# Kernel optimization log

Measured on AMD Instinct MI355X. Metric: run time of the kernel, lower is better.

Reference implementation:

```python
import jax, jax.numpy as jnp
import numpy as np

KS = 3
N = KS * KS  # 9 kernel taps
EPS = 1e-5
LEAK = 0.1


def _conv2d(x, w, b=None, stride=1, pad=1):
    out = jax.lax.conv_general_dilated(
        x, w, (stride, stride), [(pad, pad), (pad, pad)],
        dimension_numbers=('NCHW', 'OIHW', 'NCHW'))
    if b is not None:
        out = out + b[None, :, None, None]
    return out


def setup_inputs() -> dict:
    key = jax.random.key(0)
    k1, k2, k3, k4 = jax.random.split(key, 4)
    b, c_in, c_out, H, W = 4, 128, 256, 128, 128
    x = jax.random.normal(k1, (b, c_in, H, W), dtype=jnp.float32)
    # offset-predicting conv (torch inits it to zero; small random keeps
    # sampling near-grid but nontrivial)
    p_w = jax.random.normal(k2, (2 * N, c_in, KS, KS), dtype=jnp.float32) * 0.01
    p_b = jnp.zeros((2 * N,), dtype=jnp.float32)
    # main conv weight (bias=False in DeformConv2d)
    w_conv = jax.random.normal(k3, (c_out, c_in, KS, KS), dtype=jnp.float32) * 0.05
    gamma = jnp.ones((c_out,), dtype=jnp.float32)
    beta = jnp.zeros((c_out,), dtype=jnp.float32)
    return {"x": x, "p_w": p_w, "p_b": p_b, "w_conv": w_conv,
            "gamma": gamma, "beta": beta}


def reference(x, p_w, p_b, w_conv, gamma, beta):
    b, c, H, W = x.shape
    # offsets: (b, 2N, H, W); first N channels = x-offsets, last N = y-offsets
    off = jnp.transpose(_conv2d(x, p_w, p_b), (0, 2, 3, 1))  # (b,h,w,2N)
    off_x, off_y = off[..., :N], off[..., N:]

    x_pad = jnp.pad(x, ((0, 0), (0, 0), (1, 1), (1, 1)))  # zero_padding(1)
    Hp, Wp = H + 2, W + 2

    # p = p_0 + p_n + offset (in padded coordinates)
    dx = jnp.repeat(jnp.arange(-1, 2), KS).astype(x.dtype)  # (9,)
    dy = jnp.tile(jnp.arange(-1, 2), KS).astype(x.dtype)
    p0x = jnp.arange(1, H + 1, dtype=x.dtype)[None, :, None, None]
    p0y = jnp.arange(1, W + 1, dtype=x.dtype)[None, None, :, None]
    px = p0x + dx + off_x  # (b,h,w,N)
    py = p0y + dy + off_y

    fx, fy = jnp.floor(px), jnp.floor(py)
    qlt_x = jnp.clip(fx, 0, Hp - 1)
    qlt_y = jnp.clip(fy, 0, Wp - 1)
    qrb_x = jnp.clip(fx + 1, 0, Hp - 1)
    qrb_y = jnp.clip(fy + 1, 0, Wp - 1)

    pcx = jnp.clip(px, 0, Hp - 1)
    pcy = jnp.clip(py, 0, Wp - 1)

    # bilinear weights (matches original g_lt/g_rb/g_lb/g_rt)
    g_lt = (1 + (qlt_x - pcx)) * (1 + (qlt_y - pcy))
    g_rb = (1 - (qrb_x - pcx)) * (1 - (qrb_y - pcy))
    g_lb = (1 + (qlt_x - pcx)) * (1 - (qrb_y - pcy))
    g_rt = (1 - (qrb_x - pcx)) * (1 + (qlt_y - pcy))

    x_flat = x_pad.reshape(b, c, Hp * Wp)
    ilt_x, ilt_y = qlt_x.astype(jnp.int32), qlt_y.astype(jnp.int32)
    irb_x, irb_y = qrb_x.astype(jnp.int32), qrb_y.astype(jnp.int32)

    def samp(ix, iy, g):
        idx = (ix * Wp + iy).reshape(b, -1)  # (b, h*w*N)
        v = jnp.take_along_axis(x_flat, idx[:, None, :], axis=2)
        return g[:, None] * v.reshape(b, c, H, W, N)

    x_off = (samp(ilt_x, ilt_y, g_lt) + samp(irb_x, irb_y, g_rb)
             + samp(ilt_x, irb_y, g_lb) + samp(irb_x, ilt_y, g_rt))

    # equivalent to reshaping to (b,c,3h,3w) and conv(k=3,s=3), bias=False
    out = jnp.einsum('bchwn,ocn->bohw', x_off,
                     w_conv.reshape(w_conv.shape[0], c, N))

    # BatchNorm2d (training-mode batch stats, biased var) + LeakyReLU(0.1)
    mean = out.mean(axis=(0, 2, 3), keepdims=True)
    var = ((out - mean) ** 2).mean(axis=(0, 2, 3), keepdims=True)
    out = (out - mean) * jax.lax.rsqrt(var + EPS)
    out = out * gamma[None, :, None, None] + beta[None, :, None, None]
    return jnp.where(out >= 0, out, LEAK * out)
```

## Files before the change

### kernel.cpp

```cpp
#include <hip/hip_runtime.h>
#include <cstdint>

typedef __attribute__((ext_vector_type(8))) short bf16x8;
typedef __attribute__((ext_vector_type(4))) float f32x4;

#define B_   4
#define C_   128
#define H_   128
#define W_   128
#define HP_  130
#define WP_  130
#define O_   256
#define HW_  (H_*W_)

#define XPAD_BYTES   (B_*HP_*WP_*C_*2)
#define OFF_BYTE     XPAD_BYTES
#define OFF_BYTES    (B_*HW_*18*4)
#define WREPB_BYTE   (OFF_BYTE + OFF_BYTES)
#define WREPB_BYTES  (9*C_*O_*2)
#define STATS_BYTE   (WREPB_BYTE + WREPB_BYTES)
#define WOFF_BYTE    (STATS_BYTE + 4096)
#define WOFF_BYTES   (9*4*4*32*8*2)

typedef __attribute__((address_space(1))) const void gconst_void;
typedef __attribute__((address_space(3))) void lds_void;
#define GLD_LDS16(gp, lp) __builtin_amdgcn_global_load_lds((gconst_void*)(gp), (lds_void*)(lp), 16, 0, 0)

__device__ __forceinline__ unsigned pack_bf2(float a, float b) {
    unsigned ua = __builtin_bit_cast(unsigned, a) + 0x8000u;
    unsigned ub = __builtin_bit_cast(unsigned, b) + 0x8000u;
    return __builtin_amdgcn_perm(ub, ua, 0x07060302u);
}

__global__ void k_transpose(const float* __restrict__ x, unsigned short* __restrict__ xpad) {
    __shared__ float tile[32][33];
    int w0 = blockIdx.x * 32, c0 = blockIdx.y * 32;
    int bh = blockIdx.z;
    int b = bh >> 7, h = bh & 127;
    int tx = threadIdx.x, ty = threadIdx.y;
#pragma unroll
    for (int i = 0; i < 4; i++) {
        int c = c0 + ty + i * 8;
        tile[ty + i * 8][tx] = x[((b * C_ + c) * H_ + h) * W_ + w0 + tx];
    }
    __syncthreads();
    int tid = ty * 32 + tx;
    int cp = tid & 15;
    int wl = tid >> 4;
#pragma unroll
    for (int i = 0; i < 2; i++) {
        int wll = wl + i * 16;
        int w = w0 + wll;
        unsigned v = pack_bf2(tile[2 * cp][wll], tile[2 * cp + 1][wll]);
        *(unsigned*)(&xpad[((size_t)((b * HP_ + h + 1) * WP_ + (w + 1))) * C_ + c0 + 2 * cp]) = v;
    }
}

__global__ void k_repackA(const float* __restrict__ p_w, short* __restrict__ wofff,
                          const float* __restrict__ w_conv, unsigned short* __restrict__ wrepb) {
    int i = blockIdx.x * 256 + threadIdx.x;
    if (i < 9 * 4096) {
        int e = i & 7, m = (i >> 3) & 31, q = (i >> 8) & 3, kc = (i >> 10) & 3, tap = i >> 12;
        float f = (m < 18) ? p_w[((size_t)m * C_ + kc * 32 + q * 8 + e) * 9 + tap] : 0.f;
        unsigned u = __builtin_bit_cast(unsigned, f);
        u += 0x7fffu + ((u >> 16) & 1u);
        wofff[i] = (short)(u >> 16);
    }
    int j = i - 9 * 4096;
    if (j >= 0 && j < 9 * C_ * O_) {
        int ki8 = j & 7;
        int o   = (j >> 3) & 255;
        int kq  = (j >> 11) & 3;
        int kc  = (j >> 13) & 3;
        int n   = j >> 15;
        int c = kc * 32 + kq * 8 + ki8;
        float f = w_conv[(o * C_ + c) * 9 + n];
        unsigned u = __builtin_bit_cast(unsigned, f);
        u += 0x7fffu + ((u >> 16) & 1u);
        wrepb[j] = (unsigned short)(u >> 16);
    }
}

__global__ __launch_bounds__(256) void k_offconv(const unsigned short* __restrict__ xpad,
                                                 const short* __restrict__ wofff,
                                                 const float* __restrict__ p_b,
                                                 float* __restrict__ offT) {
    int t = threadIdx.x;
    int ph = blockIdx.x;
    int h  = blockIdx.y;
    int b  = blockIdx.z;
    const unsigned short* xb = xpad + (size_t)b * HP_ * WP_ * C_;
    int lane = t & 63, wv = t >> 6;
    int q = lane >> 4, l15 = lane & 15;
    int pos0 = ph * 64 + wv * 16;
    int poscol = pos0 + l15;

    f32x4 accA = {0.f, 0.f, 0.f, 0.f}, accB = {0.f, 0.f, 0.f, 0.f};
    const bf16x8* Wf = (const bf16x8*)wofff;

    for (int tap = 0; tap < 9; tap++) {
        int row = h + tap / 3;
        int col = poscol + tap % 3;
        const unsigned short* src = xb + ((size_t)(row * WP_ + col)) * C_ + q * 8;
#pragma unroll
        for (int kc = 0; kc < 4; kc++) {
            bf16x8 a0 = Wf[(size_t)(((tap * 4 + kc) * 4 + q) * 32) + l15];
            bf16x8 a1 = Wf[(size_t)(((tap * 4 + kc) * 4 + q) * 32) + 16 + l15];
            bf16x8 bv = *(const bf16x8*)(src + kc * 32);
            accA = __builtin_amdgcn_mfma_f32_16x16x32_bf16(a0, bv, accA, 0, 0, 0);
            accB = __builtin_amdgcn_mfma_f32_16x16x32_bf16(a1, bv, accB, 0, 0, 0);
        }
    }
    size_t hw = (size_t)h * W_ + pos0 + l15;
#pragma unroll
    for (int r = 0; r < 4; r++) {
        int j = q * 4 + r;
        offT[((size_t)(b * 18 + j)) * HW_ + hw] = accA[r] + p_b[j];
    }
    if (q == 0) {
#pragma unroll
        for (int r = 0; r < 2; r++) {
            int j = 16 + r;
            offT[((size_t)(b * 18 + j)) * HW_ + hw] = accB[r] + p_b[j];
        }
    }
}

__global__ __launch_bounds__(512, 4) void k_main(const unsigned short* __restrict__ xpad,
                                                 const float* __restrict__ offT,
                                                 const unsigned short* __restrict__ wrepb,
                                                 float* __restrict__ out,
                                                 float* __restrict__ stats) {
    __shared__ short Wl[2][8192];
    __shared__ short Vl[2][4128];
    __shared__ int   pbase[2][4][128];
    __shared__ float pg[2][4][128];
    __shared__ float red0[256], red1[256];

    int t = threadIdx.x;
    int i_blk = blockIdx.x;
    int b = i_blk & 3;
    int h = i_blk >> 2;
    const unsigned short* xb = xpad + (size_t)b * HP_ * WP_ * C_;

    int lane = t & 63, wv = t >> 6;
    int q = lane >> 4, l15 = lane & 15;
    int m0 = (wv & 3) * 64;
    int ph = wv >> 2;
    int n0 = ph * 64;
    int c4g = t & 3, posb = t >> 2;

    auto OFFSETS = [&](int n, int pb) {
        if (t < 128) {
            int w = t;
            float offx = offT[((size_t)(b * 18 + n)) * HW_ + h * W_ + w];
            float offy = offT[((size_t)(b * 18 + 9 + n)) * HW_ + h * W_ + w];
            int dxn = n / 3 - 1, dyn = n % 3 - 1;
            float px = (float)(h + 1 + dxn) + offx;
            float py = (float)(w + 1 + dyn) + offy;
            float pcx = fminf(fmaxf(px, 0.f), 129.f);
            float pcy = fminf(fmaxf(py, 0.f), 129.f);
            float fx = floorf(px), fy = floorf(py);
            float q0x = fminf(fmaxf(fx, 0.f), 129.f);
            float q0y = fminf(fmaxf(fy, 0.f), 129.f);
            float q1x = fminf(fmaxf(fx + 1.f, 0.f), 129.f);
            float q1y = fminf(fmaxf(fy + 1.f, 0.f), 129.f);
            float wx0 = 1.f + (q0x - pcx), wx1 = 1.f - (q1x - pcx);
            float wy0 = 1.f + (q0y - pcy), wy1 = 1.f - (q1y - pcy);
            int i0x = (int)q0x, i0y = (int)q0y, i1x = (int)q1x, i1y = (int)q1y;
            pbase[pb][0][w] = (i0x * WP_ + i0y) * C_;
            pbase[pb][1][w] = (i1x * WP_ + i1y) * C_;
            pbase[pb][2][w] = (i0x * WP_ + i1y) * C_;
            pbase[pb][3][w] = (i1x * WP_ + i0y) * C_;
            pg[pb][0][w] = wx0 * wy0;
            pg[pb][1][w] = wx1 * wy1;
            pg[pb][2][w] = wx0 * wy1;
            pg[pb][3][w] = wx1 * wy0;
        }
    };

    f32x4 acc[4][4];
#pragma unroll
    for (int i = 0; i < 4; i++)
#pragma unroll
        for (int j = 0; j < 4; j++) acc[i][j] = (f32x4){0.f, 0.f, 0.f, 0.f};

    if (t < 256) { red0[t] = 0.f; red1[t] = 0.f; }
    OFFSETS(0, 0);
    __syncthreads();

    {
        const unsigned short* ws = wrepb;
        GLD_LDS16(ws + (size_t)t * 8, &Wl[0][wv * 512]);
        GLD_LDS16(ws + (size_t)(t + 512) * 8, &Wl[0][wv * 512 + 4096]);
        int cof = c4g * 8;
        uint4 A  = *(const uint4*)(xb + pbase[0][0][posb] + cof);
        uint4 Bv = *(const uint4*)(xb + pbase[0][1][posb] + cof);
        uint4 Cv = *(const uint4*)(xb + pbase[0][2][posb] + cof);
        uint4 Dv = *(const uint4*)(xb + pbase[0][3][posb] + cof);
        float g0 = pg[0][0][posb], g1 = pg[0][1][posb], g2 = pg[0][2][posb], g3 = pg[0][3][posb];
        unsigned outw[4];
#pragma unroll
        for (int k = 0; k < 4; k++) {
            unsigned ua = (&A.x)[k], ub = (&Bv.x)[k], uc = (&Cv.x)[k], ud = (&Dv.x)[k];
            float alo = __builtin_bit_cast(float, ua << 16), ahi = __builtin_bit_cast(float, ua & 0xffff0000u);
            float blo = __builtin_bit_cast(float, ub << 16), bhi = __builtin_bit_cast(float, ub & 0xffff0000u);
            float clo = __builtin_bit_cast(float, uc << 16), chi = __builtin_bit_cast(float, uc & 0xffff0000u);
            float dlo = __builtin_bit_cast(float, ud << 16), dhi = __builtin_bit_cast(float, ud & 0xffff0000u);
            float vlo = g0 * alo + g1 * blo + g2 * clo + g3 * dlo;
            float vhi = g0 * ahi + g1 * bhi + g2 * chi + g3 * dhi;
            outw[k] = pack_bf2(vlo, vhi);
        }
        *(uint4*)&Vl[0][(unsigned)(c4g * 129 + posb) * 8] = make_uint4(outw[0], outw[1], outw[2], outw[3]);
    }
    __syncthreads();

#pragma unroll 1
    for (int s = 0; s < 36; s++) {
        int cur = s & 1, nxt = cur ^ 1;
        uint4 A, Bv, Cv, Dv;
        float g0 = 0.f, g1 = 0.f, g2 = 0.f, g3 = 0.f;
        bool st = (s < 35);
        if (st) {
            int s1 = s + 1;
            const unsigned short* ws = wrepb + (size_t)s1 * 8192;
            GLD_LDS16(ws + (size_t)t * 8, &Wl[nxt][wv * 512]);
            GLD_LDS16(ws + (size_t)(t + 512) * 8, &Wl[nxt][wv * 512 + 4096]);
            int n1 = s1 >> 2, kc1 = s1 & 3, pb1 = n1 & 1;
            int cof = kc1 * 32 + c4g * 8;
            A  = *(const uint4*)(xb + pbase[pb1][0][posb] + cof);
            Bv = *(const uint4*)(xb + pbase[pb1][1][posb] + cof);
            Cv = *(const uint4*)(xb + pbase[pb1][2][posb] + cof);
            Dv = *(const uint4*)(xb + pbase[pb1][3][posb] + cof);
            g0 = pg[pb1][0][posb]; g1 = pg[pb1][1][posb];
            g2 = pg[pb1][2][posb]; g3 = pg[pb1][3][posb];
        }
        {
            const bf16x8* Af = (const bf16x8*)Wl[cur];
            const bf16x8* Bf = (const bf16x8*)Vl[cur];
            bf16x8 av[4];
#pragma unroll
            for (int i = 0; i < 4; i++) av[i] = Af[q * 256 + m0 + i * 16 + l15];
            __builtin_amdgcn_s_setprio(1);
#pragma unroll
            for (int j = 0; j < 4; j++) {
                bf16x8 bv = Bf[q * 129 + n0 + j * 16 + l15];
#pragma unroll
                for (int i = 0; i < 4; i++)
                    acc[i][j] = __builtin_amdgcn_mfma_f32_16x16x32_bf16(av[i], bv, acc[i][j], 0, 0, 0);
            }
            __builtin_amdgcn_s_setprio(0);
        }
        if ((s & 3) == 2) {
            int n = s >> 2;
            if (n < 8) OFFSETS(n + 1, (n + 1) & 1);
        }
        if (st) {
            unsigned outw[4];
#pragma unroll
            for (int k = 0; k < 4; k++) {
                unsigned ua = (&A.x)[k], ub = (&Bv.x)[k], uc = (&Cv.x)[k], ud = (&Dv.x)[k];
                float alo = __builtin_bit_cast(float, ua << 16), ahi = __builtin_bit_cast(float, ua & 0xffff0000u);
                float blo = __builtin_bit_cast(float, ub << 16), bhi = __builtin_bit_cast(float, ub & 0xffff0000u);
                float clo = __builtin_bit_cast(float, uc << 16), chi = __builtin_bit_cast(float, uc & 0xffff0000u);
                float dlo = __builtin_bit_cast(float, ud << 16), dhi = __builtin_bit_cast(float, ud & 0xffff0000u);
                float vlo = g0 * alo + g1 * blo + g2 * clo + g3 * dlo;
                float vhi = g0 * ahi + g1 * bhi + g2 * chi + g3 * dhi;
                outw[k] = pack_bf2(vlo, vhi);
            }
            *(uint4*)&Vl[nxt][(unsigned)(c4g * 129 + posb) * 8] = make_uint4(outw[0], outw[1], outw[2], outw[3]);
        }
        __syncthreads();
    }

#pragma unroll
    for (int i = 0; i < 4; i++) {
#pragma unroll
        for (int r = 0; r < 4; r++) {
            int o_loc = m0 + i * 16 + q * 4 + r;
            float s = 0.f, s2 = 0.f;
#pragma unroll
            for (int j = 0; j < 4; j++) { float v = acc[i][j][r]; s += v; s2 += v * v; }
            s  += __shfl_xor(s, 1);  s  += __shfl_xor(s, 2);  s  += __shfl_xor(s, 4);  s  += __shfl_xor(s, 8);
            s2 += __shfl_xor(s2, 1); s2 += __shfl_xor(s2, 2); s2 += __shfl_xor(s2, 4); s2 += __shfl_xor(s2, 8);
            if (l15 == 0) { atomicAdd(&red0[o_loc], s); atomicAdd(&red1[o_loc], s2); }
        }
    }
    __syncthreads();
    if (t < 256) {
        atomicAdd(&stats[t], red0[t]);
        atomicAdd(&stats[256 + t], red1[t]);
    }

    float* outb = out + ((size_t)b * O_) * HW_ + (size_t)h * W_;
#pragma unroll
    for (int i = 0; i < 4; i++)
#pragma unroll
        for (int j = 0; j < 4; j++) {
            int col = ph * 64 + j * 16 + l15;
#pragma unroll
            for (int r = 0; r < 4; r++) {
                int o = m0 + i * 16 + q * 4 + r;
                outb[(size_t)o * HW_ + col] = acc[i][j][r];
            }
        }
}

__global__ void k_bnstats(float* __restrict__ stats,
                          const float* __restrict__ gamma,
                          const float* __restrict__ beta) {
    int t = threadIdx.x;
    float s = stats[t], s2 = stats[256 + t];
    float mean = s * (1.f / 65536.f);
    float var = s2 * (1.f / 65536.f) - mean * mean;
    float sc = gamma[t] * rsqrtf(var + 1e-5f);
    float sh = beta[t] - mean * sc;
    stats[512 + t] = sc;
    stats[768 + t] = sh;
}

__global__ __launch_bounds__(256) void k_apply(float* __restrict__ out,
                                               const float* __restrict__ stats) {
    int idx = blockIdx.x * 256 + threadIdx.x;
    int e = idx * 4;
    int o = (e >> 14) & 255;
    float sc = stats[512 + o], sh = stats[768 + o];
    float4 v = *(float4*)(out + e);
    v.x = v.x * sc + sh; v.x = (v.x >= 0.f) ? v.x : 0.1f * v.x;
    v.y = v.y * sc + sh; v.y = (v.y >= 0.f) ? v.y : 0.1f * v.y;
    v.z = v.z * sc + sh; v.z = (v.z >= 0.f) ? v.z : 0.1f * v.z;
    v.w = v.w * sc + sh; v.w = (v.w >= 0.f) ? v.w : 0.1f * v.w;
    *(float4*)(out + e) = v;
}

extern "C" void kernel_launch(void* const* d_in, const int* in_sizes, int n_in,
                              void* d_out, int out_size, void* d_ws, size_t ws_size,
                              hipStream_t stream) {
    const float* x      = (const float*)d_in[0];
    const float* p_w    = (const float*)d_in[1];
    const float* p_b    = (const float*)d_in[2];
    const float* w_conv = (const float*)d_in[3];
    const float* gamma  = (const float*)d_in[4];
    const float* beta   = (const float*)d_in[5];
    float* out = (float*)d_out;

    char* wsb = (char*)d_ws;
    unsigned short* xpad  = (unsigned short*)wsb;
    float*          offT  = (float*)(wsb + OFF_BYTE);
    unsigned short* wrepb = (unsigned short*)(wsb + WREPB_BYTE);
    float*          stats = (float*)(wsb + STATS_BYTE);
    short*          wofff = (short*)(wsb + WOFF_BYTE);

    hipMemsetAsync(xpad, 0, (size_t)XPAD_BYTES, stream);
    hipMemsetAsync(stats, 0, 4096, stream);

    k_transpose<<<dim3(W_ / 32, C_ / 32, B_ * H_), dim3(32, 8), 0, stream>>>(x, xpad);
    k_repackA<<<dim3((9 * 4096 + 9 * C_ * O_ + 255) / 256), 256, 0, stream>>>(p_w, wofff, w_conv, wrepb);
    k_offconv<<<dim3(2, H_, B_), 256, 0, stream>>>(xpad, wofff, p_b, offT);
    k_main<<<dim3(512), 512, 0, stream>>>(xpad, offT, wrepb, out, stats);
    k_bnstats<<<1, 256, 0, stream>>>(stats, gamma, beta);
    k_apply<<<dim3(16384), 256, 0, stream>>>(out, stats);
}
```

Measured before the change: 228.5 us.

## Fold padding zeroing, stats reset and BN finalize into existing kernels

Drops the full-buffer memset of the padded bf16 input: the transpose kernel now writes the zero halo rows, columns and corners itself, and it stores 16-byte vectors of eight channels instead of 4-byte pairs. The stats reset moves into the weight-repack kernel, and the BN scale/shift computation is done per thread inside the apply kernel, which removes the single-block bnstats launch. This cuts two memsets and one kernel launch plus the redundant zero-fill traffic. In exchange each apply thread recomputes the rsqrt, and correctness now depends on the halo writes covering every padded cell.

Measured after the change: 218.0 us. 4.6% less time.

```diff
diff --git a/kernel.cpp b/kernel.cpp
--- a/kernel.cpp
+++ b/kernel.cpp
@@ -43,22 +43,42 @@
         int c = c0 + ty + i * 8;
         tile[ty + i * 8][tx] = x[((b * C_ + c) * H_ + h) * W_ + w0 + tx];
     }
+    int tid = ty * 32 + tx;
+    if (h == 0) {
+        int wloc = tid >> 3, cq = tid & 7;
+        size_t r0 = ((size_t)(b * HP_ + 0)   * WP_ + (w0 + 1 + wloc)) * C_ + c0 + cq * 4;
+        size_t r1 = ((size_t)(b * HP_ + 129) * WP_ + (w0 + 1 + wloc)) * C_ + c0 + cq * 4;
+        *(uint2*)&xpad[r0] = make_uint2(0u, 0u);
+        *(uint2*)&xpad[r1] = make_uint2(0u, 0u);
+        if (w0 == 0 && tid < 128) {
+            int corner = tid >> 5, cc = tid & 31;
+            int hp = (corner & 1) ? 129 : 0;
+            int wp = (corner & 2) ? 129 : 0;
+            xpad[((size_t)(b * HP_ + hp) * WP_ + wp) * C_ + c0 + cc] = 0;
+        }
+    }
+    if (w0 == 0 && tid < 64) {
+        int side = tid >> 5, cc = tid & 31;
+        int wp = side ? 129 : 0;
+        xpad[((size_t)(b * HP_ + h + 1) * WP_ + wp) * C_ + c0 + cc] = 0;
+    }
     __syncthreads();
-    int tid = ty * 32 + tx;
-    int cp = tid & 15;
-    int wl = tid >> 4;
-#pragma unroll
-    for (int i = 0; i < 2; i++) {
-        int wll = wl + i * 16;
-        int w = w0 + wll;
-        unsigned v = pack_bf2(tile[2 * cp][wll], tile[2 * cp + 1][wll]);
-        *(unsigned*)(&xpad[((size_t)((b * HP_ + h + 1) * WP_ + (w + 1))) * C_ + c0 + 2 * cp]) = v;
+    if (tid < 128) {
+        int w = tid >> 2, u4 = tid & 3;
+        unsigned r0 = pack_bf2(tile[8 * u4 + 0][w], tile[8 * u4 + 1][w]);
+        unsigned r1 = pack_bf2(tile[8 * u4 + 2][w], tile[8 * u4 + 3][w]);
+        unsigned r2 = pack_bf2(tile[8 * u4 + 4][w], tile[8 * u4 + 5][w]);
+        unsigned r3 = pack_bf2(tile[8 * u4 + 6][w], tile[8 * u4 + 7][w]);
+        *(uint4*)&xpad[((size_t)((b * HP_ + h + 1) * WP_ + (w0 + w + 1))) * C_ + c0 + u4 * 8] =
+            make_uint4(r0, r1, r2, r3);
     }
 }
 
 __global__ void k_repackA(const float* __restrict__ p_w, short* __restrict__ wofff,
-                          const float* __restrict__ w_conv, unsigned short* __restrict__ wrepb) {
+                          const float* __restrict__ w_conv, unsigned short* __restrict__ wrepb,
+                          float* __restrict__ stats) {
     int i = blockIdx.x * 256 + threadIdx.x;
+    if (i < 1024) stats[i] = 0.f;
     if (i < 9 * 4096) {
         int e = i & 7, m = (i >> 3) & 31, q = (i >> 8) & 3, kc = (i >> 10) & 3, tap = i >> 12;
         float f = (m < 18) ? p_w[((size_t)m * C_ + kc * 32 + q * 8 + e) * 9 + tap] : 0.f;
@@ -306,25 +326,18 @@
         }
 }
 
-__global__ void k_bnstats(float* __restrict__ stats,
-                          const float* __restrict__ gamma,
-                          const float* __restrict__ beta) {
-    int t = threadIdx.x;
-    float s = stats[t], s2 = stats[256 + t];
-    float mean = s * (1.f / 65536.f);
-    float var = s2 * (1.f / 65536.f) - mean * mean;
-    float sc = gamma[t] * rsqrtf(var + 1e-5f);
-    float sh = beta[t] - mean * sc;
-    stats[512 + t] = sc;
-    stats[768 + t] = sh;
-}
-
 __global__ __launch_bounds__(256) void k_apply(float* __restrict__ out,
-                                               const float* __restrict__ stats) {
+                                               const float* __restrict__ stats,
+                                               const float* __restrict__ gamma,
+                                               const float* __restrict__ beta) {
     int idx = blockIdx.x * 256 + threadIdx.x;
     int e = idx * 4;
     int o = (e >> 14) & 255;
-    float sc = stats[512 + o], sh = stats[768 + o];
+    float s0 = stats[o], s2v = stats[256 + o];
+    float mean = s0 * (1.f / 65536.f);
+    float var = s2v * (1.f / 65536.f) - mean * mean;
+    float sc = gamma[o] * rsqrtf(var + 1e-5f);
+    float sh = beta[o] - mean * sc;
     float4 v = *(float4*)(out + e);
     v.x = v.x * sc + sh; v.x = (v.x >= 0.f) ? v.x : 0.1f * v.x;
     v.y = v.y * sc + sh; v.y = (v.y >= 0.f) ? v.y : 0.1f * v.y;
@@ -351,13 +364,9 @@
     float*          stats = (float*)(wsb + STATS_BYTE);
     short*          wofff = (short*)(wsb + WOFF_BYTE);
 
-    hipMemsetAsync(xpad, 0, (size_t)XPAD_BYTES, stream);
-    hipMemsetAsync(stats, 0, 4096, stream);
-
     k_transpose<<<dim3(W_ / 32, C_ / 32, B_ * H_), dim3(32, 8), 0, stream>>>(x, xpad);
-    k_repackA<<<dim3((9 * 4096 + 9 * C_ * O_ + 255) / 256), 256, 0, stream>>>(p_w, wofff, w_conv, wrepb);
+    k_repackA<<<dim3((9 * 4096 + 9 * C_ * O_ + 255) / 256), 256, 0, stream>>>(p_w, wofff, w_conv, wrepb, stats);
     k_offconv<<<dim3(2, H_, B_), 256, 0, stream>>>(xpad, wofff, p_b, offT);
     k_main<<<dim3(512), 512, 0, stream>>>(xpad, offT, wrepb, out, stats);
-    k_bnstats<<<1, 256, 0, stream>>>(stats, gamma, beta);
-    k_apply<<<dim3(16384), 256, 0, stream>>>(out, stats);
-}
+    k_apply<<<dim3(16384), 256, 0, stream>>>(out, stats, gamma, beta);
+}
```
